# Kernel optimization log

Hardware: AMD Instinct MI355X
Metric: run time of the kernel (lower is better)

The kernel has to match this reference:

```python
import jax, jax.numpy as jnp
import numpy as np

EPS = 1e-7  # K.epsilon()
ROUTINGS = 3
N_PRIMARY = 16384
PRIMARY_DIM = 8
NUM_CLASSES = 10
CAPSULE_DIM = 16
BATCH = 64


def squash(x):
    sn = jnp.sum(jnp.square(x), axis=-1, keepdims=True)
    return sn / (1.0 + sn) / jnp.sqrt(sn + EPS) * x


def setup_inputs() -> dict:
    key = jax.random.key(0)
    k1, k2 = jax.random.split(key)
    inputs = jax.random.normal(k1, (BATCH, N_PRIMARY, PRIMARY_DIM), dtype=jnp.float32)
    # glorot uniform over shape (1, N, C, D, dc); we store as (N, C, D, dc)
    fan_in, fan_out = PRIMARY_DIM, CAPSULE_DIM
    limit = np.sqrt(6.0 / (fan_in + fan_out))
    W = jax.random.uniform(k2, (N_PRIMARY, NUM_CLASSES, PRIMARY_DIM, CAPSULE_DIM),
                           minval=-limit, maxval=limit, dtype=jnp.float32)
    return {"inputs": inputs, "W": W}


def reference(inputs, W):
    # u_hat[b,n,c,e] = sum_d inputs[b,n,d] * W[n,c,d,e]  (true batched matmul,
    # equivalent to the tile+multiply+sum in the original)
    u_hat = jnp.einsum('bnd,ncde->bnce', inputs, W)
    B, N, C, _ = u_hat.shape
    b = jnp.zeros((B, N, C), dtype=u_hat.dtype)
    v = None
    for i in range(ROUTINGS):
        c = jax.nn.softmax(b, axis=-1)                      # [B,N,C]
        s = jnp.einsum('bnc,bnce->bce', c, u_hat)           # [B,C,dc]
        v = squash(s)                                       # [B,C,dc]
        if i < ROUTINGS - 1:
            b = b + jnp.einsum('bnce,bce->bnc', u_hat, v)   # agreement
    return v
```

## Files before the change

### kernel.cpp

```cpp
#include <hip/hip_runtime.h>
#include <cstdint>
#include <cstddef>

#define B_ 64
#define N_ 16384
#define C_ 10
#define D_ 8
#define E_ 16
#define NTB_ 4
#define NCHK_ 4
#define NPB_ (NTB_ * NCHK_)
#define GRID_ (N_ / NPB_)
#define SVOL_ (B_ * C_ * E_)
#define NP2_ 16
#define WNU_ 640

typedef __attribute__((ext_vector_type(8))) short short8;
typedef __attribute__((ext_vector_type(4))) float f32x4;
typedef __attribute__((ext_vector_type(4))) uint32_t u32x4;

__device__ __forceinline__ uint32_t pack2(float lo, float hi) {
  uint32_t r;
  asm("v_cvt_pk_bf16_f32 %0, %1, %2" : "=v"(r) : "v"(lo), "v"(hi));
  return r;
}

__device__ __forceinline__ void gload16(const uint32_t* g, uint32_t* l) {
  __builtin_amdgcn_global_load_lds(
      (const __attribute__((address_space(1))) uint32_t*)g,
      (__attribute__((address_space(3))) uint32_t*)l, 16, 0, 0);
}

__global__ __launch_bounds__(256) void convert_w_kernel(
    const float* __restrict__ W, uint32_t* __restrict__ Wb)
{
  int i4 = blockIdx.x * 256 + threadIdx.x;
  int n = i4 / 160, r4 = i4 - n * 160;
  int c = r4 >> 4, e = r4 & 15;
  const float* src = W + (size_t)(n * C_ + c) * 128 + e;
  u32x4 v;
  v[0] = pack2(src[0],  src[16]);
  v[1] = pack2(src[32], src[48]);
  v[2] = pack2(src[64], src[80]);
  v[3] = pack2(src[96], src[112]);
  *(u32x4*)(Wb + (size_t)n * WNU_ + r4 * 4) = v;
}

__global__ __launch_bounds__(256) void convert_x_kernel(
    const float* __restrict__ x, uint32_t* __restrict__ xc)
{
  int gi = blockIdx.x * 256 + threadIdx.x;
  int b = gi & 63, n = gi >> 6;
  const float* src = x + ((size_t)b * N_ + n) * D_;
  f32x4 lo = *(const f32x4*)src, hi = *(const f32x4*)(src + 4);
  u32x4 v;
  v[0] = pack2(lo[0], lo[1]);
  v[1] = pack2(lo[2], lo[3]);
  v[2] = pack2(hi[0], hi[1]);
  v[3] = pack2(hi[2], hi[3]);
  *(u32x4*)(xc + (size_t)gi * 4) = v;
}

template <int ITER, int PRE, int FLUSH>
__global__ __launch_bounds__(256, 2) void accum_kernel(
    const float* __restrict__ x, const float* __restrict__ W,
    const uint32_t* __restrict__ Wb, const uint32_t* __restrict__ xc,
    const float* __restrict__ vacc, float* __restrict__ sout, int ncopy)
{
  __shared__ __align__(16) uint32_t wbuf[2][NTB_ * WNU_];
  __shared__ __align__(16) uint32_t xbuf[NPB_ * B_ * 4];

  const int tid = threadIdx.x;
  const int lane = tid & 63;
  const int wv = tid >> 6;
  const int l15 = lane & 15;
  const int kg = lane >> 4;
  const int n0 = blockIdx.x * NPB_;
  const int b = wv * 16 + l15;

  const short8 kzero = (short8){0, 0, 0, 0, 0, 0, 0, 0};
  const f32x4 fzero = (f32x4){0.f, 0.f, 0.f, 0.f};

  f32x4 vf[C_];
  if (ITER) {
#pragma unroll
    for (int c = 0; c < C_; ++c)
      vf[c] = *(const f32x4*)&vacc[(b * C_ + c) * E_ + kg * 4];
  }

  f32x4 acc[C_];
#pragma unroll
  for (int c = 0; c < C_; ++c) acc[c] = fzero;

  if (PRE) {
    const uint32_t* src = xc + (size_t)n0 * 256;
#pragma unroll
    for (int j = 0; j < 4; ++j) {
      int u = wv * 4 + j;
      gload16(src + u * 256 + lane * 4, &xbuf[u * 256]);
    }
  } else {
#pragma unroll
    for (int it = 0; it < 8; ++it) {
      int gidx = it * 256 + tid;
      int bb = gidx >> 5, q = gidx & 31, nn2 = q >> 1, dh = q & 1;
      f32x4 v4 = *(const f32x4*)(x + (size_t)bb * (N_ * D_) +
                                 (size_t)(n0 + nn2) * D_ + dh * 4);
      int base = (nn2 * B_ + bb) * 4 + dh * 2;
      xbuf[base] = pack2(v4[0], v4[1]);
      xbuf[base + 1] = pack2(v4[2], v4[3]);
    }
  }

  auto stage_w = [&](int pb, int nbase) {
    if (PRE) {
      const uint32_t* src = Wb + (size_t)nbase * WNU_;
#pragma unroll
      for (int k = 0; k < 3; ++k) {
        int u = wv + 4 * k;
        if (u < 10) gload16(src + u * 256 + lane * 4, &wbuf[pb][u * 256]);
      }
    } else {
#pragma unroll
      for (int it = 0; it < 10; ++it) {
        int i = it * 256 + tid;
        int n = i / 640, r = i - n * 640;
        int c = r >> 6, r2 = r & 63;
        int d2 = r2 >> 4, e = r2 & 15;
        const float* p = W + ((size_t)(nbase + n) * C_ + c) * 128 + d2 * 32 + e;
        wbuf[pb][n * WNU_ + (c * E_ + e) * 4 + d2] = pack2(p[0], p[16]);
      }
    }
  };

  stage_w(0, n0);
  __syncthreads();

  for (int ch = 0; ch < NCHK_; ++ch) {
    if (ch + 1 < NCHK_) stage_w((ch + 1) & 1, n0 + (ch + 1) * NTB_);
    const uint32_t* wb = wbuf[ch & 1];

    const int nl = ch * NTB_ + kg;
    short8 xq = *(const short8*)&xbuf[(nl * B_ + b) * 4];

    if (ITER == 0) {
#pragma unroll
      for (int c = 0; c < C_; ++c) {
        short8 wfq = *(const short8*)&wb[kg * WNU_ + (c * E_ + l15) * 4];
        acc[c] = __builtin_amdgcn_mfma_f32_16x16x32_bf16(wfq, xq, acc[c], 0, 0, 0);
      }
    } else {
      short8 xm0 = (kg == 0) ? xq : kzero;
      short8 xm1 = (kg == 1) ? xq : kzero;
      short8 xm2 = (kg == 2) ? xq : kzero;
      short8 xm3 = (kg == 3) ? xq : kzero;
      const bool bb0 = (kg & 1) != 0;
      const bool bb1 = (kg & 2) != 0;

      float ew[C_];
#pragma unroll
      for (int c = 0; c < C_; ++c) {
        short8 wfq = *(const short8*)&wb[kg * WNU_ + (c * E_ + l15) * 4];
        f32x4 u0 = __builtin_amdgcn_mfma_f32_16x16x32_bf16(wfq, xm0, fzero, 0, 0, 0);
        f32x4 u1 = __builtin_amdgcn_mfma_f32_16x16x32_bf16(wfq, xm1, fzero, 0, 0, 0);
        f32x4 u2 = __builtin_amdgcn_mfma_f32_16x16x32_bf16(wfq, xm2, fzero, 0, 0, 0);
        f32x4 u3 = __builtin_amdgcn_mfma_f32_16x16x32_bf16(wfq, xm3, fzero, 0, 0, 0);
        f32x4 v = vf[c];
        float t0 = u0[0] * v[0] + u0[1] * v[1] + u0[2] * v[2] + u0[3] * v[3];
        float t1 = u1[0] * v[0] + u1[1] * v[1] + u1[2] * v[2] + u1[3] * v[3];
        float t2 = u2[0] * v[0] + u2[1] * v[1] + u2[2] * v[2] + u2[3] * v[3];
        float t3 = u3[0] * v[0] + u3[1] * v[1] + u3[2] * v[2] + u3[3] * v[3];
        float keep_lo = bb0 ? t1 : t0, send_lo = bb0 ? t0 : t1;
        float keep_hi = bb0 ? t3 : t2, send_hi = bb0 ? t2 : t3;
        float ulo = keep_lo + __shfl_xor(send_lo, 16);
        float uhi = keep_hi + __shfl_xor(send_hi, 16);
        float keep2 = bb1 ? uhi : ulo, send2 = bb1 ? ulo : uhi;
        float logit = keep2 + __shfl_xor(send2, 32);
        ew[c] = __expf(logit);
      }
      float s01 = ew[0] + ew[1], s23 = ew[2] + ew[3], s45 = ew[4] + ew[5],
            s67 = ew[6] + ew[7], s89 = ew[8] + ew[9];
      float inv = __builtin_amdgcn_rcpf(((s01 + s23) + (s45 + s67)) + s89);

      float xf[D_];
#pragma unroll
      for (int j = 0; j < D_; ++j) {
        uint32_t hw = (uint32_t)(uint16_t)xq[j];
        xf[j] = __builtin_bit_cast(float, hw << 16);
      }
#pragma unroll
      for (int c = 0; c < C_; ++c) {
        float cw = ew[c] * inv;
        u32x4 bw;
        bw[0] = pack2(cw * xf[0], cw * xf[1]);
        bw[1] = pack2(cw * xf[2], cw * xf[3]);
        bw[2] = pack2(cw * xf[4], cw * xf[5]);
        bw[3] = pack2(cw * xf[6], cw * xf[7]);
        short8 bfrag = __builtin_bit_cast(short8, bw);
        short8 wfq = *(const short8*)&wb[kg * WNU_ + (c * E_ + l15) * 4];
        acc[c] = __builtin_amdgcn_mfma_f32_16x16x32_bf16(wfq, bfrag, acc[c], 0, 0, 0);
      }
    }
    __syncthreads();
  }

  const float scale = (ITER == 0) ? 0.1f : 1.0f;
  if (FLUSH == 1) {
    f32x4* sc = (f32x4*)(sout + (size_t)blockIdx.x * SVOL_);
#pragma unroll
    for (int c = 0; c < C_; ++c) {
      f32x4 v = acc[c];
      v[0] *= scale; v[1] *= scale; v[2] *= scale; v[3] *= scale;
      sc[(b * C_ + c) * 4 + kg] = v;
    }
  } else {
    float* sc = sout + (size_t)(blockIdx.x & (ncopy - 1)) * SVOL_;
#pragma unroll
    for (int c = 0; c < C_; ++c)
#pragma unroll
      for (int r = 0; r < 4; ++r)
        atomicAdd(&sc[(b * C_ + c) * E_ + kg * 4 + r], acc[c][r] * scale);
  }
}

__global__ __launch_bounds__(256) void reduce_kernel(
    const float* __restrict__ parts, float* __restrict__ out16)
{
  int j = blockIdx.x / (SVOL_ / 256);
  int seg = blockIdx.x % (SVOL_ / 256);
  int t = seg * 256 + threadIdx.x;
  float s = 0.f;
#pragma unroll 8
  for (int k = j * (GRID_ / NP2_); k < (j + 1) * (GRID_ / NP2_); ++k)
    s += parts[(size_t)k * SVOL_ + t];
  out16[(size_t)j * SVOL_ + t] = s;
}

template <int MODE, int REZERO>
__global__ __launch_bounds__(256) void squash_kernel(
    float* __restrict__ scopy, int np,
    float* __restrict__ vacc, float* __restrict__ out)
{
  int t = blockIdx.x * 256 + threadIdx.x;
  float sv = 0.f;
  for (int k = 0; k < np; ++k) {
    sv += scopy[(size_t)k * SVOL_ + t];
    if (REZERO && MODE != 2) scopy[(size_t)k * SVOL_ + t] = 0.f;
  }
  float sq = sv * sv;
  sq += __shfl_xor(sq, 1);
  sq += __shfl_xor(sq, 2);
  sq += __shfl_xor(sq, 4);
  sq += __shfl_xor(sq, 8);
  float scale = sq / (1.f + sq) * rsqrtf(sq + 1e-7f);
  float v = scale * sv;
  if (MODE == 0)      vacc[t] = v;
  else if (MODE == 1) vacc[t] += v;
  else                out[t] = v;
}

extern "C" void kernel_launch(void* const* d_in, const int* in_sizes, int n_in,
                              void* d_out, int out_size, void* d_ws, size_t ws_size,
                              hipStream_t stream)
{
  const float* x = (const float*)d_in[0];
  const float* W = (const float*)d_in[1];
  float* out = (float*)d_out;

  const size_t WB_SZ = (size_t)N_ * WNU_ * 4;
  const size_t XC_SZ = (size_t)N_ * B_ * 4 * 4;
  const size_t PARTS_SZ = (size_t)GRID_ * SVOL_ * 4;
  const size_t TAIL_SZ = (size_t)(NP2_ + 1) * SVOL_ * 4;
  const int RB = NP2_ * (SVOL_ / 256);

  if (ws_size >= WB_SZ + XC_SZ + PARTS_SZ + TAIL_SZ) {
    uint32_t* Wb = (uint32_t*)d_ws;
    uint32_t* xcv = (uint32_t*)((char*)d_ws + WB_SZ);
    float* parts = (float*)((char*)d_ws + WB_SZ + XC_SZ);
    float* out16 = parts + (size_t)GRID_ * SVOL_;
    float* vacc = out16 + (size_t)NP2_ * SVOL_;

    convert_w_kernel<<<N_ * 160 / 256, 256, 0, stream>>>(W, Wb);
    convert_x_kernel<<<N_ * B_ / 256, 256, 0, stream>>>(x, xcv);

    accum_kernel<0, 1, 1><<<GRID_, 256, 0, stream>>>(x, W, Wb, xcv, vacc, parts, 0);
    reduce_kernel<<<RB, 256, 0, stream>>>(parts, out16);
    squash_kernel<0, 0><<<SVOL_ / 256, 256, 0, stream>>>(out16, NP2_, vacc, out);

    accum_kernel<1, 1, 1><<<GRID_, 256, 0, stream>>>(x, W, Wb, xcv, vacc, parts, 0);
    reduce_kernel<<<RB, 256, 0, stream>>>(parts, out16);
    squash_kernel<1, 0><<<SVOL_ / 256, 256, 0, stream>>>(out16, NP2_, vacc, out);

    accum_kernel<1, 1, 1><<<GRID_, 256, 0, stream>>>(x, W, Wb, xcv, vacc, parts, 0);
    reduce_kernel<<<RB, 256, 0, stream>>>(parts, out16);
    squash_kernel<2, 0><<<SVOL_ / 256, 256, 0, stream>>>(out16, NP2_, vacc, out);
  } else if (ws_size >= PARTS_SZ + TAIL_SZ) {
    float* parts = (float*)d_ws;
    float* out16 = parts + (size_t)GRID_ * SVOL_;
    float* vacc = out16 + (size_t)NP2_ * SVOL_;

    accum_kernel<0, 0, 1><<<GRID_, 256, 0, stream>>>(x, W, nullptr, nullptr, vacc, parts, 0);
    reduce_kernel<<<RB, 256, 0, stream>>>(parts, out16);
    squash_kernel<0, 0><<<SVOL_ / 256, 256, 0, stream>>>(out16, NP2_, vacc, out);

    accum_kernel<1, 0, 1><<<GRID_, 256, 0, stream>>>(x, W, nullptr, nullptr, vacc, parts, 0);
    reduce_kernel<<<RB, 256, 0, stream>>>(parts, out16);
    squash_kernel<1, 0><<<SVOL_ / 256, 256, 0, stream>>>(out16, NP2_, vacc, out);

    accum_kernel<1, 0, 1><<<GRID_, 256, 0, stream>>>(x, W, nullptr, nullptr, vacc, parts, 0);
    reduce_kernel<<<RB, 256, 0, stream>>>(parts, out16);
    squash_kernel<2, 0><<<SVOL_ / 256, 256, 0, stream>>>(out16, NP2_, vacc, out);
  } else {
    int ncopy = 64;
    while (ncopy > 1 && (size_t)(ncopy + 1) * SVOL_ * 4 > ws_size) ncopy >>= 1;
    float* s_ws = (float*)d_ws;
    float* vacc = s_ws + (size_t)ncopy * SVOL_;
    hipMemsetAsync(s_ws, 0, (size_t)ncopy * SVOL_ * 4, stream);

    accum_kernel<0, 0, 0><<<GRID_, 256, 0, stream>>>(x, W, nullptr, nullptr, vacc, s_ws, ncopy);
    squash_kernel<0, 1><<<SVOL_ / 256, 256, 0, stream>>>(s_ws, ncopy, vacc, out);

    accum_kernel<1, 0, 0><<<GRID_, 256, 0, stream>>>(x, W, nullptr, nullptr, vacc, s_ws, ncopy);
    squash_kernel<1, 1><<<SVOL_ / 256, 256, 0, stream>>>(s_ws, ncopy, vacc, out);

    accum_kernel<1, 0, 0><<<GRID_, 256, 0, stream>>>(x, W, nullptr, nullptr, vacc, s_ws, ncopy);
    squash_kernel<2, 1><<<SVOL_ / 256, 256, 0, stream>>>(s_ws, ncopy, vacc, out);
  }
}
```

Measured before the change: 158.8 us.

## Fuse bf16 conversion into first routing pass and merge reduce with squash

The standalone W and x bf16 conversion kernels are removed. The first routing pass now reads fp32 inputs, computes, and writes the packed bf16 copies to workspace for the later passes. Per-block chunk count doubles, so there are half as many partial blocks, and the two-stage reduce plus squash becomes one reduce_squash kernel that sums all partials directly. This cuts kernel launches and one full pass over W and x, at the cost of a heavier first pass with scattered global writes and a longer serial reduction per thread.

```diff
diff --git a/kernel.cpp b/kernel.cpp
--- a/kernel.cpp
+++ b/kernel.cpp
@@ -8,11 +8,10 @@
 #define D_ 8
 #define E_ 16
 #define NTB_ 4
-#define NCHK_ 4
+#define NCHK_ 8
 #define NPB_ (NTB_ * NCHK_)
 #define GRID_ (N_ / NPB_)
 #define SVOL_ (B_ * C_ * E_)
-#define NP2_ 16
 #define WNU_ 640
 
 typedef __attribute__((ext_vector_type(8))) short short8;
@@ -31,41 +30,11 @@
       (__attribute__((address_space(3))) uint32_t*)l, 16, 0, 0);
 }
 
-__global__ __launch_bounds__(256) void convert_w_kernel(
-    const float* __restrict__ W, uint32_t* __restrict__ Wb)
-{
-  int i4 = blockIdx.x * 256 + threadIdx.x;
-  int n = i4 / 160, r4 = i4 - n * 160;
-  int c = r4 >> 4, e = r4 & 15;
-  const float* src = W + (size_t)(n * C_ + c) * 128 + e;
-  u32x4 v;
-  v[0] = pack2(src[0],  src[16]);
-  v[1] = pack2(src[32], src[48]);
-  v[2] = pack2(src[64], src[80]);
-  v[3] = pack2(src[96], src[112]);
-  *(u32x4*)(Wb + (size_t)n * WNU_ + r4 * 4) = v;
-}
-
-__global__ __launch_bounds__(256) void convert_x_kernel(
-    const float* __restrict__ x, uint32_t* __restrict__ xc)
-{
-  int gi = blockIdx.x * 256 + threadIdx.x;
-  int b = gi & 63, n = gi >> 6;
-  const float* src = x + ((size_t)b * N_ + n) * D_;
-  f32x4 lo = *(const f32x4*)src, hi = *(const f32x4*)(src + 4);
-  u32x4 v;
-  v[0] = pack2(lo[0], lo[1]);
-  v[1] = pack2(lo[2], lo[3]);
-  v[2] = pack2(hi[0], hi[1]);
-  v[3] = pack2(hi[2], hi[3]);
-  *(u32x4*)(xc + (size_t)gi * 4) = v;
-}
-
-template <int ITER, int PRE, int FLUSH>
-__global__ __launch_bounds__(256, 2) void accum_kernel(
+template <int WB, int FLUSH>
+__global__ __launch_bounds__(256, 2) void pass0_kernel(
     const float* __restrict__ x, const float* __restrict__ W,
-    const uint32_t* __restrict__ Wb, const uint32_t* __restrict__ xc,
-    const float* __restrict__ vacc, float* __restrict__ sout, int ncopy)
+    uint32_t* __restrict__ Wb, uint32_t* __restrict__ xc,
+    float* __restrict__ sout, int ncopy)
 {
   __shared__ __align__(16) uint32_t wbuf[2][NTB_ * WNU_];
   __shared__ __align__(16) uint32_t xbuf[NPB_ * B_ * 4];
@@ -78,15 +47,101 @@
   const int n0 = blockIdx.x * NPB_;
   const int b = wv * 16 + l15;
 
+  f32x4 acc[C_];
+#pragma unroll
+  for (int c = 0; c < C_; ++c) acc[c] = (f32x4){0.f, 0.f, 0.f, 0.f};
+
+#pragma unroll
+  for (int it = 0; it < 16; ++it) {
+    int gidx = it * 256 + tid;
+    int bb = gidx >> 6, q = gidx & 63, nn2 = q >> 1, dh = q & 1;
+    f32x4 v4 = *(const f32x4*)(x + (size_t)bb * (N_ * D_) +
+                               (size_t)(n0 + nn2) * D_ + dh * 4);
+    uint32_t p0 = pack2(v4[0], v4[1]);
+    uint32_t p1 = pack2(v4[2], v4[3]);
+    int base = (nn2 * B_ + bb) * 4 + dh * 2;
+    xbuf[base] = p0;
+    xbuf[base + 1] = p1;
+    if (WB) {
+      uint32_t* dst = xc + (size_t)(n0 + nn2) * 256 + bb * 4 + dh * 2;
+      dst[0] = p0;
+      dst[1] = p1;
+    }
+  }
+
+  auto stage_w = [&](int pb, int nbase) {
+#pragma unroll
+    for (int it = 0; it < 10; ++it) {
+      int i = it * 256 + tid;
+      int n = i / 640, r = i - n * 640;
+      int c = r >> 6, r2 = r & 63;
+      int d2 = r2 >> 4, e = r2 & 15;
+      const float* p = W + ((size_t)(nbase + n) * C_ + c) * 128 + d2 * 32 + e;
+      uint32_t val = pack2(p[0], p[16]);
+      int fi = (c * E_ + e) * 4 + d2;
+      wbuf[pb][n * WNU_ + fi] = val;
+      if (WB) Wb[(size_t)(nbase + n) * WNU_ + fi] = val;
+    }
+  };
+
+  stage_w(0, n0);
+  __syncthreads();
+
+  for (int ch = 0; ch < NCHK_; ++ch) {
+    if (ch + 1 < NCHK_) stage_w((ch + 1) & 1, n0 + (ch + 1) * NTB_);
+    const uint32_t* wb = wbuf[ch & 1];
+    const int nl = ch * NTB_ + kg;
+    short8 xq = *(const short8*)&xbuf[(nl * B_ + b) * 4];
+#pragma unroll
+    for (int c = 0; c < C_; ++c) {
+      short8 wfq = *(const short8*)&wb[kg * WNU_ + (c * E_ + l15) * 4];
+      acc[c] = __builtin_amdgcn_mfma_f32_16x16x32_bf16(wfq, xq, acc[c], 0, 0, 0);
+    }
+    __syncthreads();
+  }
+
+  if (FLUSH == 1) {
+    f32x4* sc = (f32x4*)(sout + (size_t)blockIdx.x * SVOL_);
+#pragma unroll
+    for (int c = 0; c < C_; ++c) {
+      f32x4 v = acc[c];
+      v[0] *= 0.1f; v[1] *= 0.1f; v[2] *= 0.1f; v[3] *= 0.1f;
+      sc[(b * C_ + c) * 4 + kg] = v;
+    }
+  } else {
+    float* sc = sout + (size_t)(blockIdx.x & (ncopy - 1)) * SVOL_;
+#pragma unroll
+    for (int c = 0; c < C_; ++c)
+#pragma unroll
+      for (int r = 0; r < 4; ++r)
+        atomicAdd(&sc[(b * C_ + c) * E_ + kg * 4 + r], acc[c][r] * 0.1f);
+  }
+}
+
+template <int PRE, int FLUSH>
+__global__ __launch_bounds__(256, 2) void accum_kernel(
+    const float* __restrict__ x, const float* __restrict__ W,
+    const uint32_t* __restrict__ Wb, const uint32_t* __restrict__ xc,
+    const float* __restrict__ vacc, float* __restrict__ sout, int ncopy)
+{
+  __shared__ __align__(16) uint32_t wbuf[2][NTB_ * WNU_];
+  __shared__ __align__(16) uint32_t xbuf[NPB_ * B_ * 4];
+
+  const int tid = threadIdx.x;
+  const int lane = tid & 63;
+  const int wv = tid >> 6;
+  const int l15 = lane & 15;
+  const int kg = lane >> 4;
+  const int n0 = blockIdx.x * NPB_;
+  const int b = wv * 16 + l15;
+
   const short8 kzero = (short8){0, 0, 0, 0, 0, 0, 0, 0};
   const f32x4 fzero = (f32x4){0.f, 0.f, 0.f, 0.f};
 
   f32x4 vf[C_];
-  if (ITER) {
-#pragma unroll
-    for (int c = 0; c < C_; ++c)
-      vf[c] = *(const f32x4*)&vacc[(b * C_ + c) * E_ + kg * 4];
-  }
+#pragma unroll
+  for (int c = 0; c < C_; ++c)
+    vf[c] = *(const f32x4*)&vacc[(b * C_ + c) * E_ + kg * 4];
 
   f32x4 acc[C_];
 #pragma unroll
@@ -95,15 +150,15 @@
   if (PRE) {
     const uint32_t* src = xc + (size_t)n0 * 256;
 #pragma unroll
-    for (int j = 0; j < 4; ++j) {
-      int u = wv * 4 + j;
+    for (int j = 0; j < 8; ++j) {
+      int u = wv * 8 + j;
       gload16(src + u * 256 + lane * 4, &xbuf[u * 256]);
     }
   } else {
 #pragma unroll
-    for (int it = 0; it < 8; ++it) {
+    for (int it = 0; it < 16; ++it) {
       int gidx = it * 256 + tid;
-      int bb = gidx >> 5, q = gidx & 31, nn2 = q >> 1, dh = q & 1;
+      int bb = gidx >> 6, q = gidx & 63, nn2 = q >> 1, dh = q & 1;
       f32x4 v4 = *(const f32x4*)(x + (size_t)bb * (N_ * D_) +
                                  (size_t)(n0 + nn2) * D_ + dh * 4);
       int base = (nn2 * B_ + bb) * 4 + dh * 2;
@@ -143,110 +198,83 @@
     const int nl = ch * NTB_ + kg;
     short8 xq = *(const short8*)&xbuf[(nl * B_ + b) * 4];
 
-    if (ITER == 0) {
-#pragma unroll
-      for (int c = 0; c < C_; ++c) {
-        short8 wfq = *(const short8*)&wb[kg * WNU_ + (c * E_ + l15) * 4];
-        acc[c] = __builtin_amdgcn_mfma_f32_16x16x32_bf16(wfq, xq, acc[c], 0, 0, 0);
-      }
-    } else {
-      short8 xm0 = (kg == 0) ? xq : kzero;
-      short8 xm1 = (kg == 1) ? xq : kzero;
-      short8 xm2 = (kg == 2) ? xq : kzero;
-      short8 xm3 = (kg == 3) ? xq : kzero;
-      const bool bb0 = (kg & 1) != 0;
-      const bool bb1 = (kg & 2) != 0;
-
-      float ew[C_];
-#pragma unroll
-      for (int c = 0; c < C_; ++c) {
-        short8 wfq = *(const short8*)&wb[kg * WNU_ + (c * E_ + l15) * 4];
-        f32x4 u0 = __builtin_amdgcn_mfma_f32_16x16x32_bf16(wfq, xm0, fzero, 0, 0, 0);
-        f32x4 u1 = __builtin_amdgcn_mfma_f32_16x16x32_bf16(wfq, xm1, fzero, 0, 0, 0);
-        f32x4 u2 = __builtin_amdgcn_mfma_f32_16x16x32_bf16(wfq, xm2, fzero, 0, 0, 0);
-        f32x4 u3 = __builtin_amdgcn_mfma_f32_16x16x32_bf16(wfq, xm3, fzero, 0, 0, 0);
-        f32x4 v = vf[c];
-        float t0 = u0[0] * v[0] + u0[1] * v[1] + u0[2] * v[2] + u0[3] * v[3];
-        float t1 = u1[0] * v[0] + u1[1] * v[1] + u1[2] * v[2] + u1[3] * v[3];
-        float t2 = u2[0] * v[0] + u2[1] * v[1] + u2[2] * v[2] + u2[3] * v[3];
-        float t3 = u3[0] * v[0] + u3[1] * v[1] + u3[2] * v[2] + u3[3] * v[3];
-        float keep_lo = bb0 ? t1 : t0, send_lo = bb0 ? t0 : t1;
-        float keep_hi = bb0 ? t3 : t2, send_hi = bb0 ? t2 : t3;
-        float ulo = keep_lo + __shfl_xor(send_lo, 16);
-        float uhi = keep_hi + __shfl_xor(send_hi, 16);
-        float keep2 = bb1 ? uhi : ulo, send2 = bb1 ? ulo : uhi;
-        float logit = keep2 + __shfl_xor(send2, 32);
-        ew[c] = __expf(logit);
-      }
-      float s01 = ew[0] + ew[1], s23 = ew[2] + ew[3], s45 = ew[4] + ew[5],
-            s67 = ew[6] + ew[7], s89 = ew[8] + ew[9];
-      float inv = __builtin_amdgcn_rcpf(((s01 + s23) + (s45 + s67)) + s89);
-
-      float xf[D_];
-#pragma unroll
-      for (int j = 0; j < D_; ++j) {
-        uint32_t hw = (uint32_t)(uint16_t)xq[j];
-        xf[j] = __builtin_bit_cast(float, hw << 16);
-      }
-#pragma unroll
-      for (int c = 0; c < C_; ++c) {
-        float cw = ew[c] * inv;
-        u32x4 bw;
-        bw[0] = pack2(cw * xf[0], cw * xf[1]);
-        bw[1] = pack2(cw * xf[2], cw * xf[3]);
-        bw[2] = pack2(cw * xf[4], cw * xf[5]);
-        bw[3] = pack2(cw * xf[6], cw * xf[7]);
-        short8 bfrag = __builtin_bit_cast(short8, bw);
-        short8 wfq = *(const short8*)&wb[kg * WNU_ + (c * E_ + l15) * 4];
-        acc[c] = __builtin_amdgcn_mfma_f32_16x16x32_bf16(wfq, bfrag, acc[c], 0, 0, 0);
-      }
+    short8 xm0 = (kg == 0) ? xq : kzero;
+    short8 xm1 = (kg == 1) ? xq : kzero;
+    short8 xm2 = (kg == 2) ? xq : kzero;
+    short8 xm3 = (kg == 3) ? xq : kzero;
+    const bool bb0 = (kg & 1) != 0;
+    const bool bb1 = (kg & 2) != 0;
+
+    float ew[C_];
+#pragma unroll
+    for (int c = 0; c < C_; ++c) {
+      short8 wfq = *(const short8*)&wb[kg * WNU_ + (c * E_ + l15) * 4];
+      f32x4 u0 = __builtin_amdgcn_mfma_f32_16x16x32_bf16(wfq, xm0, fzero, 0, 0, 0);
+      f32x4 u1 = __builtin_amdgcn_mfma_f32_16x16x32_bf16(wfq, xm1, fzero, 0, 0, 0);
+      f32x4 u2 = __builtin_amdgcn_mfma_f32_16x16x32_bf16(wfq, xm2, fzero, 0, 0, 0);
+      f32x4 u3 = __builtin_amdgcn_mfma_f32_16x16x32_bf16(wfq, xm3, fzero, 0, 0, 0);
+      f32x4 v = vf[c];
+      float t0 = u0[0] * v[0] + u0[1] * v[1] + u0[2] * v[2] + u0[3] * v[3];
+      float t1 = u1[0] * v[0] + u1[1] * v[1] + u1[2] * v[2] + u1[3] * v[3];
+      float t2 = u2[0] * v[0] + u2[1] * v[1] + u2[2] * v[2] + u2[3] * v[3];
+      float t3 = u3[0] * v[0] + u3[1] * v[1] + u3[2] * v[2] + u3[3] * v[3];
+      float keep_lo = bb0 ? t1 : t0, send_lo = bb0 ? t0 : t1;
+      float keep_hi = bb0 ? t3 : t2, send_hi = bb0 ? t2 : t3;
+      float ulo = keep_lo + __shfl_xor(send_lo, 16);
+      float uhi = keep_hi + __shfl_xor(send_hi, 16);
+      float keep2 = bb1 ? uhi : ulo, send2 = bb1 ? ulo : uhi;
+      float logit = keep2 + __shfl_xor(send2, 32);
+      ew[c] = __expf(logit);
+    }
+    float s01 = ew[0] + ew[1], s23 = ew[2] + ew[3], s45 = ew[4] + ew[5],
+          s67 = ew[6] + ew[7], s89 = ew[8] + ew[9];
+    float inv = __builtin_amdgcn_rcpf(((s01 + s23) + (s45 + s67)) + s89);
+
+    float xf[D_];
+#pragma unroll
+    for (int j = 0; j < D_; ++j) {
+      uint32_t hw = (uint32_t)(uint16_t)xq[j];
+      xf[j] = __builtin_bit_cast(float, hw << 16);
+    }
+#pragma unroll
+    for (int c = 0; c < C_; ++c) {
+      float cw = ew[c] * inv;
+      u32x4 bw;
+      bw[0] = pack2(cw * xf[0], cw * xf[1]);
+      bw[1] = pack2(cw * xf[2], cw * xf[3]);
+      bw[2] = pack2(cw * xf[4], cw * xf[5]);
+      bw[3] = pack2(cw * xf[6], cw * xf[7]);
+      short8 bfrag = __builtin_bit_cast(short8, bw);
+      short8 wfq = *(const short8*)&wb[kg * WNU_ + (c * E_ + l15) * 4];
+      acc[c] = __builtin_amdgcn_mfma_f32_16x16x32_bf16(wfq, bfrag, acc[c], 0, 0, 0);
     }
     __syncthreads();
   }
 
-  const float scale = (ITER == 0) ? 0.1f : 1.0f;
   if (FLUSH == 1) {
     f32x4* sc = (f32x4*)(sout + (size_t)blockIdx.x * SVOL_);
 #pragma unroll
-    for (int c = 0; c < C_; ++c) {
-      f32x4 v = acc[c];
-      v[0] *= scale; v[1] *= scale; v[2] *= scale; v[3] *= scale;
-      sc[(b * C_ + c) * 4 + kg] = v;
-    }
+    for (int c = 0; c < C_; ++c)
+      sc[(b * C_ + c) * 4 + kg] = acc[c];
   } else {
     float* sc = sout + (size_t)(blockIdx.x & (ncopy - 1)) * SVOL_;
 #pragma unroll
     for (int c = 0; c < C_; ++c)
 #pragma unroll
       for (int r = 0; r < 4; ++r)
-        atomicAdd(&sc[(b * C_ + c) * E_ + kg * 4 + r], acc[c][r] * scale);
-  }
-}
-
-__global__ __launch_bounds__(256) void reduce_kernel(
-    const float* __restrict__ parts, float* __restrict__ out16)
-{
-  int j = blockIdx.x / (SVOL_ / 256);
-  int seg = blockIdx.x % (SVOL_ / 256);
-  int t = seg * 256 + threadIdx.x;
-  float s = 0.f;
-#pragma unroll 8
-  for (int k = j * (GRID_ / NP2_); k < (j + 1) * (GRID_ / NP2_); ++k)
-    s += parts[(size_t)k * SVOL_ + t];
-  out16[(size_t)j * SVOL_ + t] = s;
-}
-
-template <int MODE, int REZERO>
-__global__ __launch_bounds__(256) void squash_kernel(
-    float* __restrict__ scopy, int np,
+        atomicAdd(&sc[(b * C_ + c) * E_ + kg * 4 + r], acc[c][r]);
+  }
+}
+
+template <int MODE>
+__global__ __launch_bounds__(256) void reduce_squash_kernel(
+    const float* __restrict__ parts, int np,
     float* __restrict__ vacc, float* __restrict__ out)
 {
   int t = blockIdx.x * 256 + threadIdx.x;
   float sv = 0.f;
-  for (int k = 0; k < np; ++k) {
-    sv += scopy[(size_t)k * SVOL_ + t];
-    if (REZERO && MODE != 2) scopy[(size_t)k * SVOL_ + t] = 0.f;
-  }
+#pragma unroll 8
+  for (int k = 0; k < np; ++k) sv += parts[(size_t)k * SVOL_ + t];
   float sq = sv * sv;
   sq += __shfl_xor(sq, 1);
   sq += __shfl_xor(sq, 2);
@@ -259,6 +287,29 @@
   else                out[t] = v;
 }
 
+template <int MODE>
+__global__ __launch_bounds__(256) void squash_stripes_kernel(
+    float* __restrict__ scopy, int ncopy,
+    float* __restrict__ vacc, float* __restrict__ out)
+{
+  int t = blockIdx.x * 256 + threadIdx.x;
+  float sv = 0.f;
+  for (int k = 0; k < ncopy; ++k) {
+    sv += scopy[(size_t)k * SVOL_ + t];
+    if (MODE != 2) scopy[(size_t)k * SVOL_ + t] = 0.f;
+  }
+  float sq = sv * sv;
+  sq += __shfl_xor(sq, 1);
+  sq += __shfl_xor(sq, 2);
+  sq += __shfl_xor(sq, 4);
+  sq += __shfl_xor(sq, 8);
+  float scale = sq / (1.f + sq) * rsqrtf(sq + 1e-7f);
+  float v = scale * sv;
+  if (MODE == 0)      vacc[t] = v;
+  else if (MODE == 1) vacc[t] += v;
+  else                out[t] = v;
+}
+
 extern "C" void kernel_launch(void* const* d_in, const int* in_sizes, int n_in,
                               void* d_out, int out_size, void* d_ws, size_t ws_size,
                               hipStream_t stream)
@@ -270,46 +321,34 @@
   const size_t WB_SZ = (size_t)N_ * WNU_ * 4;
   const size_t XC_SZ = (size_t)N_ * B_ * 4 * 4;
   const size_t PARTS_SZ = (size_t)GRID_ * SVOL_ * 4;
-  const size_t TAIL_SZ = (size_t)(NP2_ + 1) * SVOL_ * 4;
-  const int RB = NP2_ * (SVOL_ / 256);
-
-  if (ws_size >= WB_SZ + XC_SZ + PARTS_SZ + TAIL_SZ) {
+  const size_t VACC_SZ = (size_t)SVOL_ * 4;
+
+  if (ws_size >= WB_SZ + XC_SZ + PARTS_SZ + VACC_SZ) {
     uint32_t* Wb = (uint32_t*)d_ws;
     uint32_t* xcv = (uint32_t*)((char*)d_ws + WB_SZ);
     float* parts = (float*)((char*)d_ws + WB_SZ + XC_SZ);
-    float* out16 = parts + (size_t)GRID_ * SVOL_;
-    float* vacc = out16 + (size_t)NP2_ * SVOL_;
-
-    convert_w_kernel<<<N_ * 160 / 256, 256, 0, stream>>>(W, Wb);
-    convert_x_kernel<<<N_ * B_ / 256, 256, 0, stream>>>(x, xcv);
-
-    accum_kernel<0, 1, 1><<<GRID_, 256, 0, stream>>>(x, W, Wb, xcv, vacc, parts, 0);
-    reduce_kernel<<<RB, 256, 0, stream>>>(parts, out16);
-    squash_kernel<0, 0><<<SVOL_ / 256, 256, 0, stream>>>(out16, NP2_, vacc, out);
-
-    accum_kernel<1, 1, 1><<<GRID_, 256, 0, stream>>>(x, W, Wb, xcv, vacc, parts, 0);
-    reduce_kernel<<<RB, 256, 0, stream>>>(parts, out16);
-    squash_kernel<1, 0><<<SVOL_ / 256, 256, 0, stream>>>(out16, NP2_, vacc, out);
-
-    accum_kernel<1, 1, 1><<<GRID_, 256, 0, stream>>>(x, W, Wb, xcv, vacc, parts, 0);
-    reduce_kernel<<<RB, 256, 0, stream>>>(parts, out16);
-    squash_kernel<2, 0><<<SVOL_ / 256, 256, 0, stream>>>(out16, NP2_, vacc, out);
-  } else if (ws_size >= PARTS_SZ + TAIL_SZ) {
+    float* vacc = parts + (size_t)GRID_ * SVOL_;
+
+    pass0_kernel<1, 1><<<GRID_, 256, 0, stream>>>(x, W, Wb, xcv, parts, 0);
+    reduce_squash_kernel<0><<<SVOL_ / 256, 256, 0, stream>>>(parts, GRID_, vacc, out);
+
+    accum_kernel<1, 1><<<GRID_, 256, 0, stream>>>(x, W, Wb, xcv, vacc, parts, 0);
+    reduce_squash_kernel<1><<<SVOL_ / 256, 256, 0, stream>>>(parts, GRID_, vacc, out);
+
+    accum_kernel<1, 1><<<GRID_, 256, 0, stream>>>(x, W, Wb, xcv, vacc, parts, 0);
+    reduce_squash_kernel<2><<<SVOL_ / 256, 256, 0, stream>>>(parts, GRID_, vacc, out);
+  } else if (ws_size >= PARTS_SZ + VACC_SZ) {
     float* parts = (float*)d_ws;
-    float* out16 = parts + (size_t)GRID_ * SVOL_;
-    float* vacc = out16 + (size_t)NP2_ * SVOL_;
-
-    accum_kernel<0, 0, 1><<<GRID_, 256, 0, stream>>>(x, W, nullptr, nullptr, vacc, parts, 0);
-    reduce_kernel<<<RB, 256, 0, stream>>>(parts, out16);
-    squash_kernel<0, 0><<<SVOL_ / 256, 256, 0, stream>>>(out16, NP2_, vacc, out);
-
-    accum_kernel<1, 0, 1><<<GRID_, 256, 0, stream>>>(x, W, nullptr, nullptr, vacc, parts, 0);
-    reduce_kernel<<<RB, 256, 0, stream>>>(parts, out16);
-    squash_kernel<1, 0><<<SVOL_ / 256, 256, 0, stream>>>(out16, NP2_, vacc, out);
-
-    accum_kernel<1, 0, 1><<<GRID_, 256, 0, stream>>>(x, W, nullptr, nullptr, vacc, parts, 0);
-    reduce_kernel<<<RB, 256, 0, stream>>>(parts, out16);
-    squash_kernel<2, 0><<<SVOL_ / 256, 256, 0, stream>>>(out16, NP2_, vacc, out);
+    float* vacc = parts + (size_t)GRID_ * SVOL_;
+
+    pass0_kernel<0, 1><<<GRID_, 256, 0, stream>>>(x, W, nullptr, nullptr, parts, 0);
+    reduce_squash_kernel<0><<<SVOL_ / 256, 256, 0, stream>>>(parts, GRID_, vacc, out);
+
+    accum_kernel<0, 1><<<GRID_, 256, 0, stream>>>(x, W, nullptr, nullptr, vacc, parts, 0);
+    reduce_squash_kernel<1><<<SVOL_ / 256, 256, 0, stream>>>(parts, GRID_, vacc, out);
+
+    accum_kernel<0, 1><<<GRID_, 256, 0, stream>>>(x, W, nullptr, nullptr, vacc, parts, 0);
+    reduce_squash_kernel<2><<<SVOL_ / 256, 256, 0, stream>>>(parts, GRID_, vacc, out);
   } else {
     int ncopy = 64;
     while (ncopy > 1 && (size_t)(ncopy + 1) * SVOL_ * 4 > ws_size) ncopy >>= 1;
@@ -317,13 +356,13 @@
     float* vacc = s_ws + (size_t)ncopy * SVOL_;
     hipMemsetAsync(s_ws, 0, (size_t)ncopy * SVOL_ * 4, stream);
 
-    accum_kernel<0, 0, 0><<<GRID_, 256, 0, stream>>>(x, W, nullptr, nullptr, vacc, s_ws, ncopy);
-    squash_kernel<0, 1><<<SVOL_ / 256, 256, 0, stream>>>(s_ws, ncopy, vacc, out);
-
-    accum_kernel<1, 0, 0><<<GRID_, 256, 0, stream>>>(x, W, nullptr, nullptr, vacc, s_ws, ncopy);
-    squash_kernel<1, 1><<<SVOL_ / 256, 256, 0, stream>>>(s_ws, ncopy, vacc, out);
-
-    accum_kernel<1, 0, 0><<<GRID_, 256, 0, stream>>>(x, W, nullptr, nullptr, vacc, s_ws, ncopy);
-    squash_kernel<2, 1><<<SVOL_ / 256, 256, 0, stream>>>(s_ws, ncopy, vacc, out);
-  }
-}
+    pass0_kernel<0, 0><<<GRID_, 256, 0, stream>>>(x, W, nullptr, nullptr, s_ws, ncopy);
+    squash_stripes_kernel<0><<<SVOL_ / 256, 256, 0, stream>>>(s_ws, ncopy, vacc, out);
+
+    accum_kernel<0, 0><<<GRID_, 256, 0, stream>>>(x, W, nullptr, nullptr, vacc, s_ws, ncopy);
+    squash_stripes_kernel<1><<<SVOL_ / 256, 256, 0, stream>>>(s_ws, ncopy, vacc, out);
+
+    accum_kernel<0, 0><<<GRID_, 256, 0, stream>>>(x, W, nullptr, nullptr, vacc, s_ws, ncopy);
+    squash_stripes_kernel<2><<<SVOL_ / 256, 256, 0, stream>>>(s_ws, ncopy, vacc, out);
+  }
+}
```

Result: slower. 225.3 us (+41.9%).
